# Optimization experiments

Measured on AMD Instinct MI355X. Metric: run time of the kernel, lower is better.

Reference implementation:

```python
import jax, jax.numpy as jnp
import numpy as np

EPS = 1e-05


def setup_inputs() -> dict:
    key = jax.random.key(0)
    ks = jax.random.split(key, 4)
    B, N, D, H, E = 16, 8192, 128, 64, 64
    x = jax.random.normal(ks[0], (B, N, D), dtype=jnp.float32)
    ln_w = jnp.ones((D,), jnp.float32)
    ln_b = jnp.zeros((D,), jnp.float32)
    Wl = jax.random.normal(ks[1], (D, H), dtype=jnp.float32) / np.sqrt(D)
    bl = jnp.zeros((H,), jnp.float32)
    Wr = jax.random.normal(ks[2], (D, H), dtype=jnp.float32) / np.sqrt(D)
    br = jnp.zeros((H,), jnp.float32)
    Wo = jax.random.normal(ks[3], (H, E), dtype=jnp.float32) / np.sqrt(H)
    bo = jnp.zeros((E,), jnp.float32)
    return {"x": x, "ln_w": ln_w, "ln_b": ln_b, "Wl": Wl, "bl": bl,
            "Wr": Wr, "br": br, "Wo": Wo, "bo": bo}


def _layernorm(x, w, b):
    mu = jnp.mean(x, axis=-1, keepdims=True)
    var = jnp.mean(jnp.square(x - mu), axis=-1, keepdims=True)
    return (x - mu) * jax.lax.rsqrt(var + EPS) * w + b


def reference(x, ln_w, ln_b, Wl, bl, Wr, br, Wo, bo):
    # x: [B, N, D]
    xn = _layernorm(x, ln_w, ln_b)
    left = xn @ Wl + bl    # [B, N, H]
    right = xn @ Wr + br   # [B, N, H]
    # Original: einsum('b i d, b j d -> b i j d').mean(dim=1).
    # Identical math without the O(N^2) tensor: mean over i factors out of
    # the product since left[b,i,d]*right[b,j,d] is separable in i.
    outer = left.mean(axis=1)[:, None, :] * right  # [B, N, H]
    return outer @ Wo + bo  # [B, N, E]
```

## Files before the change

### kernel.cpp

```cpp
#include <hip/hip_runtime.h>
#include <math.h>

#define B_  16
#define N_  8192
#define D_  128
#define H_  64
#define E_  64
#define EPSLN 1e-5f

#define WS_COL   0
#define WS_M     (WS_COL + B_*D_)
#define WS_T     (WS_M + B_*D_*E_)
#define WS_C     (WS_T + B_*E_)

__global__ __launch_bounds__(256) void k_stats(const float* __restrict__ x,
                                               float* __restrict__ colacc) {
    __shared__ float mul[256], rsl[256];
    int b = blockIdx.y, t = threadIdx.x;
    int rowbase = blockIdx.x * 256;
    size_t g = (size_t)(b * N_ + rowbase);

    const float4* xr = (const float4*)(x + (g + t) * D_);
    float s = 0.f, s2 = 0.f;
#pragma unroll 8
    for (int k = 0; k < 32; ++k) {
        float4 v = xr[k];
        s  += (v.x + v.y) + (v.z + v.w);
        s2 += (v.x * v.x + v.y * v.y) + (v.z * v.z + v.w * v.w);
    }
    float mu  = s * (1.f / D_);
    float var = s2 * (1.f / D_) - mu * mu;
    mul[t] = mu;
    rsl[t] = rsqrtf(var + EPSLN);
    __syncthreads();

    int c = t & 127, half = t >> 7;
    const float* xp = x + (g + half * 128) * D_ + c;
    float acc = 0.f;
#pragma unroll 8
    for (int i = 0; i < 128; ++i) {
        acc += rsl[half * 128 + i] * (xp[(size_t)i * D_] - mul[half * 128 + i]);
    }
    atomicAdd(&colacc[b * D_ + c], acc);
}

__global__ __launch_bounds__(256) void k_combine(const float* __restrict__ colacc,
                                                 const float* __restrict__ ln_w,
                                                 const float* __restrict__ ln_b,
                                                 const float* __restrict__ Wl,
                                                 const float* __restrict__ bl,
                                                 const float* __restrict__ Wr,
                                                 const float* __restrict__ br,
                                                 const float* __restrict__ Wo,
                                                 const float* __restrict__ bo,
                                                 float* __restrict__ Mg,
                                                 float* __restrict__ Tg,
                                                 float* __restrict__ Cg) {
    int b = blockIdx.y, dblk = blockIdx.x, t = threadIdx.x;
    __shared__ float cm[D_], ml[H_], uu[H_], qq[H_];
    __shared__ float P[H_ * E_];

    if (t < D_) cm[t] = ln_w[t] * colacc[b * D_ + t] * (1.f / N_) + ln_b[t];
    __syncthreads();

    if (t < H_) {
        float a = bl[t], u = 0.f, q = 0.f;
        for (int d = 0; d < D_; ++d) {
            float wr = Wr[d * H_ + t];
            a += cm[d] * Wl[d * H_ + t];
            u += ln_w[d] * wr;
            q += ln_b[d] * wr;
        }
        ml[t] = a; uu[t] = u; qq[t] = q + br[t];
    }
    __syncthreads();

#pragma unroll
    for (int k = 0; k < 16; ++k) {
        int idx = t + 256 * k;
        P[idx] = ml[idx >> 6] * Wo[idx];
    }
    __syncthreads();

    int d  = dblk * 32 + (t >> 3);
    int eo = (t & 7) * 8;
    float a0 = 0, a1 = 0, a2 = 0, a3 = 0, a4 = 0, a5 = 0, a6 = 0, a7 = 0;
    for (int h = 0; h < H_; ++h) {
        float wr = Wr[d * H_ + h];
        const float4* p4 = (const float4*)&P[h * E_ + eo];
        float4 pa = p4[0], pb = p4[1];
        a0 += wr * pa.x; a1 += wr * pa.y; a2 += wr * pa.z; a3 += wr * pa.w;
        a4 += wr * pb.x; a5 += wr * pb.y; a6 += wr * pb.z; a7 += wr * pb.w;
    }
    float wd = ln_w[d];
    float4* Mo = (float4*)&Mg[(size_t)b * D_ * E_ + d * E_ + eo];
    Mo[0] = make_float4(wd * a0, wd * a1, wd * a2, wd * a3);
    Mo[1] = make_float4(wd * a4, wd * a5, wd * a6, wd * a7);

    if (dblk == 0 && t < E_) {
        float T = 0.f, C = bo[t];
        for (int h = 0; h < H_; ++h) {
            float p = P[h * E_ + t];
            T += uu[h] * p;
            C += qq[h] * p;
        }
        Tg[b * E_ + t] = T;
        Cg[b * E_ + t] = C;
    }
}

__global__ __launch_bounds__(256, 2) void k_gemm(const float* __restrict__ x,
                                                 const float* __restrict__ Mg,
                                                 const float* __restrict__ Tg,
                                                 const float* __restrict__ Cg,
                                                 float* __restrict__ out) {
    __shared__ float Ml[D_ * E_];
    __shared__ float xt[32 * 256];
    __shared__ float Tl[E_], Cl[E_], mul[256], rsl[256];

    int b = blockIdx.y, t = threadIdx.x;
    int rowbase = blockIdx.x * 256;

    const float4* Ms = (const float4*)(Mg + (size_t)b * D_ * E_);
    float4* Md = (float4*)Ml;
#pragma unroll
    for (int k = 0; k < 8; ++k) Md[t + 256 * k] = Ms[t + 256 * k];
    if (t < E_) { Tl[t] = Tg[b * E_ + t]; Cl[t] = Cg[b * E_ + t]; }

    int wave = t >> 6, lane = t & 63;
    int tr = lane >> 3, te = lane & 7;
    int xbase = wave * 64 + tr * 8;
    int ebase = te * 8;

    size_t grow = (size_t)(b * N_ + rowbase + t);
    const float4* xrow = (const float4*)(x + grow * D_);

    float acc[8][8];
#pragma unroll
    for (int i = 0; i < 8; ++i)
#pragma unroll
        for (int j = 0; j < 8; ++j) acc[i][j] = 0.f;

    float s = 0.f, s2 = 0.f;

    for (int c = 0; c < 4; ++c) {
#pragma unroll
        for (int j = 0; j < 8; ++j) {
            float4 v = xrow[c * 8 + j];
            s  += (v.x + v.y) + (v.z + v.w);
            s2 += (v.x * v.x + v.y * v.y) + (v.z * v.z + v.w * v.w);
            xt[(j * 4 + 0) * 256 + t] = v.x;
            xt[(j * 4 + 1) * 256 + t] = v.y;
            xt[(j * 4 + 2) * 256 + t] = v.z;
            xt[(j * 4 + 3) * 256 + t] = v.w;
        }
        __syncthreads();

#pragma unroll 4
        for (int dl = 0; dl < 32; ++dl) {
            const float* xp = &xt[dl * 256 + xbase];
            float4 xa = *(const float4*)xp;
            float4 xb = *(const float4*)(xp + 4);
            const float* mp = &Ml[(c * 32 + dl) * E_ + ebase];
            float4 ma = *(const float4*)mp;
            float4 mb = *(const float4*)(mp + 4);
            float xs[8] = {xa.x, xa.y, xa.z, xa.w, xb.x, xb.y, xb.z, xb.w};
            float ms[8] = {ma.x, ma.y, ma.z, ma.w, mb.x, mb.y, mb.z, mb.w};
#pragma unroll
            for (int i = 0; i < 8; ++i)
#pragma unroll
                for (int j = 0; j < 8; ++j) acc[i][j] += xs[i] * ms[j];
        }
        __syncthreads();
    }

    {
        float mu  = s * (1.f / D_);
        float var = s2 * (1.f / D_) - mu * mu;
        mul[t] = mu;
        rsl[t] = rsqrtf(var + EPSLN);
    }
    __syncthreads();

    size_t outbase = (size_t)(b * N_ + rowbase) * E_;
#pragma unroll
    for (int i = 0; i < 8; ++i) {
        int r = xbase + i;
        float m = mul[r], rs = rsl[r];
        float4 o0, o1;
        o0.x = rs * (acc[i][0] - m * Tl[ebase + 0]) + Cl[ebase + 0];
        o0.y = rs * (acc[i][1] - m * Tl[ebase + 1]) + Cl[ebase + 1];
        o0.z = rs * (acc[i][2] - m * Tl[ebase + 2]) + Cl[ebase + 2];
        o0.w = rs * (acc[i][3] - m * Tl[ebase + 3]) + Cl[ebase + 3];
        o1.x = rs * (acc[i][4] - m * Tl[ebase + 4]) + Cl[ebase + 4];
        o1.y = rs * (acc[i][5] - m * Tl[ebase + 5]) + Cl[ebase + 5];
        o1.z = rs * (acc[i][6] - m * Tl[ebase + 6]) + Cl[ebase + 6];
        o1.w = rs * (acc[i][7] - m * Tl[ebase + 7]) + Cl[ebase + 7];
        float4* op = (float4*)&out[outbase + (size_t)r * E_ + ebase];
        op[0] = o0;
        op[1] = o1;
    }
}

extern "C" void kernel_launch(void* const* d_in, const int* in_sizes, int n_in,
                              void* d_out, int out_size, void* d_ws, size_t ws_size,
                              hipStream_t stream) {
    const float* x    = (const float*)d_in[0];
    const float* ln_w = (const float*)d_in[1];
    const float* ln_b = (const float*)d_in[2];
    const float* Wl   = (const float*)d_in[3];
    const float* bl   = (const float*)d_in[4];
    const float* Wr   = (const float*)d_in[5];
    const float* br   = (const float*)d_in[6];
    const float* Wo   = (const float*)d_in[7];
    const float* bo   = (const float*)d_in[8];
    float* out = (float*)d_out;
    float* ws  = (float*)d_ws;

    float* colacc = ws + WS_COL;
    float* Mg     = ws + WS_M;
    float* Tg     = ws + WS_T;
    float* Cg     = ws + WS_C;

    hipMemsetAsync(colacc, 0, B_ * D_ * sizeof(float), stream);

    k_stats<<<dim3(N_ / 256, B_), 256, 0, stream>>>(x, colacc);
    k_combine<<<dim3(4, B_), 256, 0, stream>>>(colacc, ln_w, ln_b, Wl, bl, Wr,
                                               br, Wo, bo, Mg, Tg, Cg);
    k_gemm<<<dim3(N_ / 256, B_), 256, 0, stream>>>(x, Mg, Tg, Cg, out);
}
```

Baseline: 169.5 us.

## Use bf16 MFMA for main GEMM and stage x tiles in LDS for stats

The main GEMM now converts x to bf16 in swizzled shared memory and computes x·M with 16x16x32 bf16 MFMA instructions, replacing the FP32 register-blocked outer product. M is stored transposed in bf16 so B fragments can be loaded straight from global memory. The stats kernel now loads 64-row tiles into padded LDS, reduces with shuffles and reads column sums from LDS rather than strided global reads. bf16 rounding of x and M lowers accuracy, and the MFMA output layout gives narrower, less coalesced stores.

```diff
diff --git a/kernel.cpp b/kernel.cpp
--- a/kernel.cpp
+++ b/kernel.cpp
@@ -8,40 +8,67 @@
 #define E_  64
 #define EPSLN 1e-5f
 
-#define WS_COL   0
-#define WS_M     (WS_COL + B_*D_)
-#define WS_T     (WS_M + B_*D_*E_)
-#define WS_C     (WS_T + B_*E_)
+typedef __attribute__((ext_vector_type(8))) short short8;
+typedef __attribute__((ext_vector_type(4))) float f32x4;
+
+#define WSB_COL 0
+#define WSB_MT  8192
+#define WSB_T   270336
+#define WSB_C   274432
+
+static __device__ __forceinline__ unsigned short f2bf(float f) {
+    union { float f; unsigned u; } c; c.f = f;
+    unsigned u = c.u;
+    return (unsigned short)((u + 0x7FFFu + ((u >> 16) & 1u)) >> 16);
+}
 
 __global__ __launch_bounds__(256) void k_stats(const float* __restrict__ x,
                                                float* __restrict__ colacc) {
-    __shared__ float mul[256], rsl[256];
+    __shared__ float xs[64 * 132];
+    __shared__ float mul[64], rsl[64], red[128];
     int b = blockIdx.y, t = threadIdx.x;
-    int rowbase = blockIdx.x * 256;
-    size_t g = (size_t)(b * N_ + rowbase);
-
-    const float4* xr = (const float4*)(x + (g + t) * D_);
-    float s = 0.f, s2 = 0.f;
-#pragma unroll 8
-    for (int k = 0; k < 32; ++k) {
-        float4 v = xr[k];
-        s  += (v.x + v.y) + (v.z + v.w);
-        s2 += (v.x * v.x + v.y * v.y) + (v.z * v.z + v.w * v.w);
-    }
-    float mu  = s * (1.f / D_);
-    float var = s2 * (1.f / D_) - mu * mu;
-    mul[t] = mu;
-    rsl[t] = rsqrtf(var + EPSLN);
-    __syncthreads();
-
-    int c = t & 127, half = t >> 7;
-    const float* xp = x + (g + half * 128) * D_ + c;
+    int rowbase = blockIdx.x * 64;
+    size_t gbase = (size_t)(b * N_ + rowbase) * 32;
+
+    const float4* x4 = (const float4*)x;
+#pragma unroll
+    for (int k = 0; k < 8; ++k) {
+        int idx = t + 256 * k;
+        int row = idx >> 5, c4 = idx & 31;
+        *(float4*)&xs[row * 132 + c4 * 4] = x4[gbase + idx];
+    }
+    __syncthreads();
+
+    {
+        int r = t >> 2, q = t & 3;
+        float s = 0.f, s2 = 0.f;
+#pragma unroll
+        for (int i = 0; i < 8; ++i) {
+            float4 v = *(const float4*)&xs[r * 132 + q * 32 + i * 4];
+            s  += (v.x + v.y) + (v.z + v.w);
+            s2 += (v.x * v.x + v.y * v.y) + (v.z * v.z + v.w * v.w);
+        }
+        s  += __shfl_xor(s, 1, 64);  s  += __shfl_xor(s, 2, 64);
+        s2 += __shfl_xor(s2, 1, 64); s2 += __shfl_xor(s2, 2, 64);
+        if (q == 0) {
+            float mu  = s * (1.f / D_);
+            float var = s2 * (1.f / D_) - mu * mu;
+            mul[r] = mu;
+            rsl[r] = rsqrtf(var + EPSLN);
+        }
+    }
+    __syncthreads();
+
+    int c = t & 127, hh = t >> 7;
     float acc = 0.f;
 #pragma unroll 8
-    for (int i = 0; i < 128; ++i) {
-        acc += rsl[half * 128 + i] * (xp[(size_t)i * D_] - mul[half * 128 + i]);
-    }
-    atomicAdd(&colacc[b * D_ + c], acc);
+    for (int i = 0; i < 32; ++i) {
+        int r = hh * 32 + i;
+        acc += rsl[r] * (xs[r * 132 + c] - mul[r]);
+    }
+    if (hh == 1) red[c] = acc;
+    __syncthreads();
+    if (hh == 0) atomicAdd(&colacc[b * D_ + c], acc + red[c]);
 }
 
 __global__ __launch_bounds__(256) void k_combine(const float* __restrict__ colacc,
@@ -53,7 +80,7 @@
                                                  const float* __restrict__ br,
                                                  const float* __restrict__ Wo,
                                                  const float* __restrict__ bo,
-                                                 float* __restrict__ Mg,
+                                                 unsigned short* __restrict__ Mt,
                                                  float* __restrict__ Tg,
                                                  float* __restrict__ Cg) {
     int b = blockIdx.y, dblk = blockIdx.x, t = threadIdx.x;
@@ -93,9 +120,15 @@
         a4 += wr * pb.x; a5 += wr * pb.y; a6 += wr * pb.z; a7 += wr * pb.w;
     }
     float wd = ln_w[d];
-    float4* Mo = (float4*)&Mg[(size_t)b * D_ * E_ + d * E_ + eo];
-    Mo[0] = make_float4(wd * a0, wd * a1, wd * a2, wd * a3);
-    Mo[1] = make_float4(wd * a4, wd * a5, wd * a6, wd * a7);
+    size_t mb = (size_t)b * E_ * D_;
+    Mt[mb + (size_t)(eo + 0) * D_ + d] = f2bf(wd * a0);
+    Mt[mb + (size_t)(eo + 1) * D_ + d] = f2bf(wd * a1);
+    Mt[mb + (size_t)(eo + 2) * D_ + d] = f2bf(wd * a2);
+    Mt[mb + (size_t)(eo + 3) * D_ + d] = f2bf(wd * a3);
+    Mt[mb + (size_t)(eo + 4) * D_ + d] = f2bf(wd * a4);
+    Mt[mb + (size_t)(eo + 5) * D_ + d] = f2bf(wd * a5);
+    Mt[mb + (size_t)(eo + 6) * D_ + d] = f2bf(wd * a6);
+    Mt[mb + (size_t)(eo + 7) * D_ + d] = f2bf(wd * a7);
 
     if (dblk == 0 && t < E_) {
         float T = 0.f, C = bo[t];
@@ -110,71 +143,35 @@
 }
 
 __global__ __launch_bounds__(256, 2) void k_gemm(const float* __restrict__ x,
-                                                 const float* __restrict__ Mg,
+                                                 const unsigned short* __restrict__ Mt,
                                                  const float* __restrict__ Tg,
                                                  const float* __restrict__ Cg,
                                                  float* __restrict__ out) {
-    __shared__ float Ml[D_ * E_];
-    __shared__ float xt[32 * 256];
-    __shared__ float Tl[E_], Cl[E_], mul[256], rsl[256];
+    __shared__ short xs[256 * 128];
+    __shared__ float mul[256], rsl[256], Tl[E_], Cl[E_];
 
     int b = blockIdx.y, t = threadIdx.x;
     int rowbase = blockIdx.x * 256;
 
-    const float4* Ms = (const float4*)(Mg + (size_t)b * D_ * E_);
-    float4* Md = (float4*)Ml;
-#pragma unroll
-    for (int k = 0; k < 8; ++k) Md[t + 256 * k] = Ms[t + 256 * k];
     if (t < E_) { Tl[t] = Tg[b * E_ + t]; Cl[t] = Cg[b * E_ + t]; }
 
-    int wave = t >> 6, lane = t & 63;
-    int tr = lane >> 3, te = lane & 7;
-    int xbase = wave * 64 + tr * 8;
-    int ebase = te * 8;
-
-    size_t grow = (size_t)(b * N_ + rowbase + t);
-    const float4* xrow = (const float4*)(x + grow * D_);
-
-    float acc[8][8];
-#pragma unroll
-    for (int i = 0; i < 8; ++i)
-#pragma unroll
-        for (int j = 0; j < 8; ++j) acc[i][j] = 0.f;
-
-    float s = 0.f, s2 = 0.f;
-
-    for (int c = 0; c < 4; ++c) {
-#pragma unroll
-        for (int j = 0; j < 8; ++j) {
-            float4 v = xrow[c * 8 + j];
-            s  += (v.x + v.y) + (v.z + v.w);
-            s2 += (v.x * v.x + v.y * v.y) + (v.z * v.z + v.w * v.w);
-            xt[(j * 4 + 0) * 256 + t] = v.x;
-            xt[(j * 4 + 1) * 256 + t] = v.y;
-            xt[(j * 4 + 2) * 256 + t] = v.z;
-            xt[(j * 4 + 3) * 256 + t] = v.w;
-        }
-        __syncthreads();
-
-#pragma unroll 4
-        for (int dl = 0; dl < 32; ++dl) {
-            const float* xp = &xt[dl * 256 + xbase];
-            float4 xa = *(const float4*)xp;
-            float4 xb = *(const float4*)(xp + 4);
-            const float* mp = &Ml[(c * 32 + dl) * E_ + ebase];
-            float4 ma = *(const float4*)mp;
-            float4 mb = *(const float4*)(mp + 4);
-            float xs[8] = {xa.x, xa.y, xa.z, xa.w, xb.x, xb.y, xb.z, xb.w};
-            float ms[8] = {ma.x, ma.y, ma.z, ma.w, mb.x, mb.y, mb.z, mb.w};
-#pragma unroll
-            for (int i = 0; i < 8; ++i)
-#pragma unroll
-                for (int j = 0; j < 8; ++j) acc[i][j] += xs[i] * ms[j];
-        }
-        __syncthreads();
-    }
-
     {
+        const float4* xrow = (const float4*)(x + (size_t)(b * N_ + rowbase + t) * D_);
+        float s = 0.f, s2 = 0.f;
+        int sw = t & 15;
+#pragma unroll
+        for (int g = 0; g < 16; ++g) {
+            float4 va = xrow[2 * g], vb = xrow[2 * g + 1];
+            s  += (va.x + va.y) + (va.z + va.w) + (vb.x + vb.y) + (vb.z + vb.w);
+            s2 += (va.x * va.x + va.y * va.y) + (va.z * va.z + va.w * va.w)
+                + (vb.x * vb.x + vb.y * vb.y) + (vb.z * vb.z + vb.w * vb.w);
+            short8 sv;
+            sv[0] = (short)f2bf(va.x); sv[1] = (short)f2bf(va.y);
+            sv[2] = (short)f2bf(va.z); sv[3] = (short)f2bf(va.w);
+            sv[4] = (short)f2bf(vb.x); sv[5] = (short)f2bf(vb.y);
+            sv[6] = (short)f2bf(vb.z); sv[7] = (short)f2bf(vb.w);
+            *(short8*)&xs[t * 128 + ((g ^ sw) * 8)] = sv;
+        }
         float mu  = s * (1.f / D_);
         float var = s2 * (1.f / D_) - mu * mu;
         mul[t] = mu;
@@ -182,23 +179,56 @@
     }
     __syncthreads();
 
+    int wv = t >> 6, lane = t & 63;
+    int m16 = lane & 15, quad = lane >> 4;
+
+    f32x4 acc[4][4];
+#pragma unroll
+    for (int i = 0; i < 4; ++i)
+#pragma unroll
+        for (int j = 0; j < 4; ++j) acc[i][j] = (f32x4){0.f, 0.f, 0.f, 0.f};
+
+    const unsigned short* Mb = Mt + (size_t)b * E_ * D_;
+
+#pragma unroll
+    for (int kc = 0; kc < 4; ++kc) {
+        short8 af[4], bf[4];
+#pragma unroll
+        for (int mt = 0; mt < 4; ++mt) {
+            int row = wv * 64 + mt * 16 + m16;
+            int g = kc * 4 + quad;
+            af[mt] = *(const short8*)&xs[row * 128 + ((g ^ m16) * 8)];
+        }
+#pragma unroll
+        for (int nt = 0; nt < 4; ++nt) {
+            bf[nt] = *(const short8*)(Mb + (size_t)(nt * 16 + m16) * D_ + kc * 32 + quad * 8);
+        }
+#pragma unroll
+        for (int mt = 0; mt < 4; ++mt)
+#pragma unroll
+            for (int nt = 0; nt < 4; ++nt)
+                acc[mt][nt] = __builtin_amdgcn_mfma_f32_16x16x32_bf16(
+                    af[mt], bf[nt], acc[mt][nt], 0, 0, 0);
+    }
+
     size_t outbase = (size_t)(b * N_ + rowbase) * E_;
 #pragma unroll
-    for (int i = 0; i < 8; ++i) {
-        int r = xbase + i;
-        float m = mul[r], rs = rsl[r];
-        float4 o0, o1;
-        o0.x = rs * (acc[i][0] - m * Tl[ebase + 0]) + Cl[ebase + 0];
-        o0.y = rs * (acc[i][1] - m * Tl[ebase + 1]) + Cl[ebase + 1];
-        o0.z = rs * (acc[i][2] - m * Tl[ebase + 2]) + Cl[ebase + 2];
-        o0.w = rs * (acc[i][3] - m * Tl[ebase + 3]) + Cl[ebase + 3];
-        o1.x = rs * (acc[i][4] - m * Tl[ebase + 4]) + Cl[ebase + 4];
-        o1.y = rs * (acc[i][5] - m * Tl[ebase + 5]) + Cl[ebase + 5];
-        o1.z = rs * (acc[i][6] - m * Tl[ebase + 6]) + Cl[ebase + 6];
-        o1.w = rs * (acc[i][7] - m * Tl[ebase + 7]) + Cl[ebase + 7];
-        float4* op = (float4*)&out[outbase + (size_t)r * E_ + ebase];
-        op[0] = o0;
-        op[1] = o1;
+    for (int mt = 0; mt < 4; ++mt) {
+        int rb = wv * 64 + mt * 16 + quad * 4;
+        float mu0 = mul[rb + 0], rs0 = rsl[rb + 0];
+        float mu1 = mul[rb + 1], rs1 = rsl[rb + 1];
+        float mu2 = mul[rb + 2], rs2 = rsl[rb + 2];
+        float mu3 = mul[rb + 3], rs3 = rsl[rb + 3];
+#pragma unroll
+        for (int nt = 0; nt < 4; ++nt) {
+            int col = nt * 16 + m16;
+            float Tc = Tl[col], Cc = Cl[col];
+            float* o = out + outbase + (size_t)rb * E_ + col;
+            o[0 * E_] = rs0 * (acc[mt][nt][0] - mu0 * Tc) + Cc;
+            o[1 * E_] = rs1 * (acc[mt][nt][1] - mu1 * Tc) + Cc;
+            o[2 * E_] = rs2 * (acc[mt][nt][2] - mu2 * Tc) + Cc;
+            o[3 * E_] = rs3 * (acc[mt][nt][3] - mu3 * Tc) + Cc;
+        }
     }
 }
 
@@ -215,17 +245,17 @@
     const float* Wo   = (const float*)d_in[7];
     const float* bo   = (const float*)d_in[8];
     float* out = (float*)d_out;
-    float* ws  = (float*)d_ws;
-
-    float* colacc = ws + WS_COL;
-    float* Mg     = ws + WS_M;
-    float* Tg     = ws + WS_T;
-    float* Cg     = ws + WS_C;
+    char* ws   = (char*)d_ws;
+
+    float*          colacc = (float*)(ws + WSB_COL);
+    unsigned short* Mt     = (unsigned short*)(ws + WSB_MT);
+    float*          Tg     = (float*)(ws + WSB_T);
+    float*          Cg     = (float*)(ws + WSB_C);
 
     hipMemsetAsync(colacc, 0, B_ * D_ * sizeof(float), stream);
 
-    k_stats<<<dim3(N_ / 256, B_), 256, 0, stream>>>(x, colacc);
+    k_stats<<<dim3(N_ / 64, B_), 256, 0, stream>>>(x, colacc);
     k_combine<<<dim3(4, B_), 256, 0, stream>>>(colacc, ln_w, ln_b, Wl, bl, Wr,
-                                               br, Wo, bo, Mg, Tg, Cg);
-    k_gemm<<<dim3(N_ / 256, B_), 256, 0, stream>>>(x, Mg, Tg, Cg, out);
-}
+                                               br, Wo, bo, Mt, Tg, Cg);
+    k_gemm<<<dim3(N_ / 256, B_), 256, 0, stream>>>(x, Mt, Tg, Cg, out);
+}
```

New measurement: 145.1 us. 14.4% less time.
